# Kernel optimization log

Measured on AMD Instinct MI355X. Metric: run time of the kernel, lower is better.

The kernel has to match this reference:

```python
import jax, jax.numpy as jnp
import numpy as np
import math

N_NODES = 100000
N_EDGES = 1600000
IN_CH = 128
EDGE_DIM = 8
HEADS = 4
C1, C2 = 10, 5  # per-head out channels of conv1/conv2
N_GRAPHS = 64


def setup_inputs() -> dict:
    key = jax.random.key(0)
    k = jax.random.split(key, 26)
    s = 0.05
    d1, d2 = HEADS * C1, HEADS * C2  # 40, 20
    lin = lambda kk, fi, fo: jax.random.normal(kk, (fi, fo), jnp.float32) * s
    inp = {}
    inp['x'] = jax.random.normal(k[0], (N_NODES, IN_CH), jnp.float32)
    inp['edge_index'] = jax.random.randint(k[1], (2, N_EDGES), 0, N_NODES)
    inp['edge_attr'] = jax.random.normal(k[2], (N_EDGES, EDGE_DIM), jnp.float32)
    inp['batch'] = jnp.sort(jax.random.randint(k[3], (N_NODES,), 0, N_GRAPHS))
    # conv1 params (TransformerConv: lin_query/key/value + lin_edge(no bias) + lin_skip)
    inp['Wq1'] = lin(k[4], IN_CH, d1); inp['bq1'] = jnp.zeros((d1,), jnp.float32)
    inp['Wk1'] = lin(k[5], IN_CH, d1); inp['bk1'] = jnp.zeros((d1,), jnp.float32)
    inp['Wv1'] = lin(k[6], IN_CH, d1); inp['bv1'] = jnp.zeros((d1,), jnp.float32)
    inp['We1'] = lin(k[7], EDGE_DIM, d1)
    inp['Ws1'] = lin(k[8], IN_CH, d1); inp['bs1'] = jnp.zeros((d1,), jnp.float32)
    # conv2 params
    inp['Wq2'] = lin(k[9], d1, d2); inp['bq2'] = jnp.zeros((d2,), jnp.float32)
    inp['Wk2'] = lin(k[10], d1, d2); inp['bk2'] = jnp.zeros((d2,), jnp.float32)
    inp['Wv2'] = lin(k[11], d1, d2); inp['bv2'] = jnp.zeros((d2,), jnp.float32)
    inp['We2'] = lin(k[12], EDGE_DIM, d2)
    inp['Ws2'] = lin(k[13], d1, d2); inp['bs2'] = jnp.zeros((d2,), jnp.float32)
    # MLP head
    inp['W1'] = lin(k[14], d2, 10); inp['b1'] = jnp.zeros((10,), jnp.float32)
    inp['W2'] = lin(k[15], 10, 3); inp['b2'] = jnp.zeros((3,), jnp.float32)
    return inp


def _segment_softmax(alpha, dst, n):
    # numerically stable softmax over incoming edges of each target node
    amax = jax.ops.segment_max(alpha, dst, num_segments=n)
    ex = jnp.exp(alpha - amax[dst])
    den = jax.ops.segment_sum(ex, dst, num_segments=n)
    return ex / (den[dst] + 1e-16)


def _transformer_conv(x, src, dst, eattr, Wq, bq, Wk, bk, Wv, bv, We, Ws, bs, heads, ch):
    n = x.shape[0]
    q = (x @ Wq + bq).reshape(n, heads, ch)
    k = (x @ Wk + bk).reshape(n, heads, ch)
    v = (x @ Wv + bv).reshape(n, heads, ch)
    e = (eattr @ We).reshape(-1, heads, ch)          # [E,H,C]
    kj = k[src] + e                                   # gather + edge bias
    alpha = jnp.einsum('ehc,ehc->eh', q[dst], kj) / math.sqrt(ch)
    alpha = _segment_softmax(alpha, dst, n)           # [E,H]
    msg = (v[src] + e) * alpha[:, :, None]
    out = jax.ops.segment_sum(msg, dst, num_segments=n).reshape(n, heads * ch)
    return out + x @ Ws + bs                          # root/skip connection (beta=False)


def reference(x, edge_index, edge_attr, batch, Wq1, bq1, Wk1, bk1, Wv1, bv1, We1, Ws1, bs1, Wq2, bq2, Wk2, bk2, Wv2, bv2, We2, Ws2, bs2, W1, b1, W2, b2):
    src, dst = edge_index[0], edge_index[1]
    h = jax.nn.relu(_transformer_conv(x, src, dst, edge_attr, Wq1, bq1, Wk1, bk1, Wv1, bv1, We1, Ws1, bs1, HEADS, C1))
    h = jax.nn.relu(_transformer_conv(h, src, dst, edge_attr, Wq2, bq2, Wk2, bk2, Wv2, bv2, We2, Ws2, bs2, HEADS, C2))
    # global_mean_pool
    sums = jax.ops.segment_sum(h, batch, num_segments=N_GRAPHS)
    cnt = jax.ops.segment_sum(jnp.ones((h.shape[0],), h.dtype), batch, num_segments=N_GRAPHS)
    pooled = sums / jnp.maximum(cnt, 1.0)[:, None]
    h = jax.nn.relu(pooled @ W1 + b1)
    return h @ W2 + b2
```

## Files before the change

### kernel.cpp

```cpp
#include <hip/hip_runtime.h>
#include <math.h>

typedef short bf16x8 __attribute__((ext_vector_type(8)));
typedef float f32x4 __attribute__((ext_vector_type(4)));

__device__ __forceinline__ unsigned bfr_(float f) {
    unsigned u = __float_as_uint(f);
    return (u + 0x7fffu + ((u >> 16) & 1u)) >> 16;
}
__device__ __forceinline__ unsigned pack2_(float lo, float hi) {
    return bfr_(lo) | (bfr_(hi) << 16);
}
__device__ __forceinline__ float unlo_(unsigned u) { return __uint_as_float(u << 16); }
__device__ __forceinline__ float unhi_(unsigned u) { return __uint_as_float(u & 0xffff0000u); }
__device__ __forceinline__ float bf2f_(unsigned short us) {
    return __uint_as_float((unsigned)us << 16);
}

__global__ void k_hist(const int* __restrict__ dst, int* __restrict__ deg, int E) {
    int e = blockIdx.x * 256 + threadIdx.x;
    if (e < E) atomicAdd(&deg[dst[e]], 1);
}

__global__ void k_scan1(const int* __restrict__ deg, int* __restrict__ rp,
                        int* __restrict__ bsum, int n) {
    __shared__ int sh[256];
    int t = threadIdx.x;
    int base = blockIdx.x * 1024 + t * 4;
    int v0 = (base + 0 < n) ? deg[base + 0] : 0;
    int v1 = (base + 1 < n) ? deg[base + 1] : 0;
    int v2 = (base + 2 < n) ? deg[base + 2] : 0;
    int v3 = (base + 3 < n) ? deg[base + 3] : 0;
    int ts = v0 + v1 + v2 + v3;
    sh[t] = ts;
    __syncthreads();
    for (int off = 1; off < 256; off <<= 1) {
        int x = (t >= off) ? sh[t - off] : 0;
        __syncthreads();
        sh[t] += x;
        __syncthreads();
    }
    int run = sh[t] - ts;
    if (base + 0 < n) rp[base + 0] = run;
    run += v0;
    if (base + 1 < n) rp[base + 1] = run;
    run += v1;
    if (base + 2 < n) rp[base + 2] = run;
    run += v2;
    if (base + 3 < n) rp[base + 3] = run;
    if (t == 255) bsum[blockIdx.x] = sh[255];
}

__global__ void k_scan2(int* __restrict__ bsum, int nb) {
    __shared__ int sh[256];
    int t = threadIdx.x;
    int v = (t < nb) ? bsum[t] : 0;
    sh[t] = v;
    __syncthreads();
    for (int off = 1; off < 256; off <<= 1) {
        int x = (t >= off) ? sh[t - off] : 0;
        __syncthreads();
        sh[t] += x;
        __syncthreads();
    }
    if (t < nb) bsum[t] = sh[t] - v;
}

__global__ void k_scan3(int* __restrict__ rp, const int* __restrict__ bsum,
                        int* __restrict__ cur, int n, int total) {
    int t = threadIdx.x;
    int base = blockIdx.x * 1024 + t * 4;
    int add = bsum[blockIdx.x];
    if (base + 0 < n) { rp[base + 0] += add; cur[base + 0] = 0; }
    if (base + 1 < n) { rp[base + 1] += add; cur[base + 1] = 0; }
    if (base + 2 < n) { rp[base + 2] += add; cur[base + 2] = 0; }
    if (base + 3 < n) { rp[base + 3] += add; cur[base + 3] = 0; }
    if (blockIdx.x == 0 && t == 0) rp[n] = total;
}

__global__ void k_scatter(const int* __restrict__ src, const int* __restrict__ dst,
                          const int* __restrict__ rp, int* __restrict__ cur,
                          const float4* __restrict__ ea, int* __restrict__ src_perm,
                          uint4* __restrict__ eap, int E) {
    int e = blockIdx.x * 256 + threadIdx.x;
    if (e >= E) return;
    float4 a = ea[(size_t)e * 2 + 0];
    float4 b = ea[(size_t)e * 2 + 1];
    uint4 u;
    u.x = pack2_(a.x, a.y);
    u.y = pack2_(a.z, a.w);
    u.z = pack2_(b.x, b.y);
    u.w = pack2_(b.z, b.w);
    int d = dst[e];
    int pos = rp[d] + atomicAdd(&cur[d], 1);
    src_perm[pos] = src[e];
    eap[pos] = u;
}

__global__ void k_wprep(const float* __restrict__ Wq, const float* __restrict__ Wk,
                        const float* __restrict__ Wv, const float* __restrict__ Ws,
                        short* __restrict__ wpackT) {
    int i = blockIdx.x * 256 + threadIdx.x;
    if (i >= 160 * 136) return;
    int c = i / 136, k = i % 136;
    short v = 0;
    if (k < 128) {
        const float* W = c < 40 ? Wq : c < 80 ? Wk : c < 120 ? Wv : Ws;
        v = (short)bfr_(W[k * 40 + (c % 40)]);
    }
    wpackT[i] = v;
}

__global__ __launch_bounds__(256) void k_proj1m(
    const float* __restrict__ X, const short* __restrict__ wpackT,
    const float* __restrict__ bq, const float* __restrict__ bk,
    const float* __restrict__ bv, const float* __restrict__ bs,
    unsigned short* __restrict__ qO, unsigned* __restrict__ kvO,
    unsigned short* __restrict__ sO, int N) {
    __shared__ short xs[64 * 136];
    __shared__ short wt[160 * 136];
    int t = threadIdx.x;
    int nb = blockIdx.x * 64;
    for (int i = t; i < 64 * 32; i += 256) {
        int nl = i >> 5, k4 = (i & 31) * 4;
        int node = nb + nl;
        float4 val = make_float4(0.f, 0.f, 0.f, 0.f);
        if (node < N) val = *(const float4*)(X + (size_t)node * 128 + k4);
        uint2 pk;
        pk.x = pack2_(val.x, val.y);
        pk.y = pack2_(val.z, val.w);
        *(uint2*)(xs + nl * 136 + k4) = pk;
    }
    {
        const uint4* wsrc = (const uint4*)wpackT;
        uint4* wdst = (uint4*)wt;
        for (int i = t; i < 2720; i += 256) wdst[i] = wsrc[i];
    }
    __syncthreads();
    int wv = t >> 6;
    int lane = t & 63;
    int lrow = lane & 15;
    int kgrp = lane >> 4;
    bf16x8 afr[4];
    const short* xbase = xs + (wv * 16 + lrow) * 136;
#pragma unroll
    for (int kk = 0; kk < 4; ++kk)
        afr[kk] = *(const bf16x8*)(xbase + kk * 32 + kgrp * 8);
    f32x4 acc[10];
#pragma unroll
    for (int nt = 0; nt < 10; ++nt) acc[nt] = (f32x4){0.f, 0.f, 0.f, 0.f};
#pragma unroll
    for (int nt = 0; nt < 10; ++nt) {
        const short* wbase = wt + (nt * 16 + lrow) * 136;
#pragma unroll
        for (int kk = 0; kk < 4; ++kk) {
            bf16x8 bfr8 = *(const bf16x8*)(wbase + kk * 32 + kgrp * 8);
            acc[nt] = __builtin_amdgcn_mfma_f32_16x16x32_bf16(afr[kk], bfr8, acc[nt],
                                                              0, 0, 0);
        }
    }
    __syncthreads();
    float* cs = (float*)wt;
#pragma unroll
    for (int nt = 0; nt < 10; ++nt)
#pragma unroll
        for (int r = 0; r < 4; ++r)
            cs[(wv * 16 + kgrp * 4 + r) * 160 + nt * 16 + lrow] = acc[nt][r];
    __syncthreads();
    for (int i = t; i < 64 * 40; i += 256) {
        int nl = i / 40, c = i % 40;
        int node = nb + nl;
        if (node < N) {
            const float* row = cs + nl * 160;
            int hh = c / 10, cc = c % 10;
            float qv = row[c] + bq[c];
            float kf = row[40 + c] + bk[c];
            float vf = row[80 + c] + bv[c];
            float sv = row[120 + c] + bs[c];
            qO[(size_t)node * 64 + hh * 16 + cc] = (unsigned short)bfr_(qv);
            kvO[(size_t)node * 64 + hh * 16 + cc] = pack2_(kf, vf);
            sO[(size_t)node * 40 + c] = (unsigned short)bfr_(sv);
        }
    }
}

template <int FIN, int CH, int KTILE, int NPT, int KVP, int QP, int NPB>
__global__ __launch_bounds__(256) void k_proj(
    const float* __restrict__ X,
    const float* __restrict__ Wq, const float* __restrict__ Wk,
    const float* __restrict__ Wv, const float* __restrict__ Ws,
    const float* __restrict__ bq, const float* __restrict__ bk,
    const float* __restrict__ bv, const float* __restrict__ bs,
    unsigned short* __restrict__ qO, unsigned* __restrict__ kvO,
    unsigned short* __restrict__ sO, int N) {
    constexpr int FOUT = 4 * CH;
    constexpr int COLS = 4 * FOUT;
    constexpr int NCG = COLS / 10;
    constexpr int NG = 256 / NCG;
    static_assert(NG * NPT == NPB, "geometry");
    constexpr int F4 = FIN / 4;
    __shared__ float xs[FIN * NPB];
    __shared__ float wbuf[KTILE * COLS];
    int t = threadIdx.x;
    int nb = blockIdx.x * NPB;
    for (int i = t; i < NPB * F4; i += 256) {
        int nl = i % NPB;
        int k4 = (i / NPB) * 4;
        int node = nb + nl;
        float4 val = make_float4(0.f, 0.f, 0.f, 0.f);
        if (node < N) val = *(const float4*)(X + (size_t)node * FIN + k4);
        xs[(k4 + 0) * NPB + nl] = val.x;
        xs[(k4 + 1) * NPB + nl] = val.y;
        xs[(k4 + 2) * NPB + nl] = val.z;
        xs[(k4 + 3) * NPB + nl] = val.w;
    }
    int cg = t % NCG, ng = t / NCG;
    int which = (cg * 10) / FOUT, cc0 = (cg * 10) % FOUT;
    float acc[NPT][10];
#pragma unroll
    for (int i = 0; i < NPT; ++i)
#pragma unroll
        for (int j = 0; j < 10; ++j) acc[i][j] = 0.f;

    for (int kt = 0; kt < FIN; kt += KTILE) {
        __syncthreads();
        for (int i = t; i < KTILE * (COLS / 4); i += 256) {
            int kk = i / (COLS / 4);
            int c4 = (i % (COLS / 4)) * 4;
            int wh = c4 / FOUT, cc = c4 % FOUT;
            const float* Wsrc = wh == 0 ? Wq : wh == 1 ? Wk : wh == 2 ? Wv : Ws;
            float4 wv = *(const float4*)(Wsrc + (size_t)(kt + kk) * FOUT + cc);
            wbuf[kk * COLS + c4 + 0] = wv.x;
            wbuf[kk * COLS + c4 + 1] = wv.y;
            wbuf[kk * COLS + c4 + 2] = wv.z;
            wbuf[kk * COLS + c4 + 3] = wv.w;
        }
        __syncthreads();
#pragma unroll 4
        for (int kk = 0; kk < KTILE; ++kk) {
            float xv[NPT];
            if constexpr (NPT == 4) {
                float4 x4 = *(const float4*)(xs + (kt + kk) * NPB + ng * 4);
                xv[0] = x4.x; xv[1] = x4.y; xv[2] = x4.z; xv[3] = x4.w;
            } else if constexpr (NPT == 2) {
                float2 x2 = *(const float2*)(xs + (kt + kk) * NPB + ng * 2);
                xv[0] = x2.x; xv[1] = x2.y;
            } else {
                xv[0] = xs[(kt + kk) * NPB + ng];
            }
            const float2* wp = (const float2*)(wbuf + kk * COLS + cg * 10);
            float wv[10];
#pragma unroll
            for (int jj = 0; jj < 5; ++jj) {
                float2 w2 = wp[jj];
                wv[2 * jj] = w2.x;
                wv[2 * jj + 1] = w2.y;
            }
#pragma unroll
            for (int i = 0; i < NPT; ++i)
#pragma unroll
                for (int j = 0; j < 10; ++j) acc[i][j] += xv[i] * wv[j];
        }
    }
    const float* B = which == 0 ? bq : which == 1 ? bk : which == 2 ? bv : bs;
    float bias[10];
#pragma unroll
    for (int j = 0; j < 10; ++j) bias[j] = B[cc0 + j];
    __syncthreads();
    if (which == 0) {
#pragma unroll
        for (int i = 0; i < NPT; ++i) {
            int node = nb + ng * NPT + i;
            if (node < N)
#pragma unroll
                for (int j = 0; j < 10; ++j) {
                    int col = cc0 + j, hh = col / CH, cc = col % CH;
                    qO[(size_t)node * 4 * QP + hh * QP + cc] =
                        (unsigned short)bfr_(acc[i][j] + bias[j]);
                }
        }
    } else if (which == 3) {
#pragma unroll
        for (int i = 0; i < NPT; ++i) {
            int node = nb + ng * NPT + i;
            if (node < N)
#pragma unroll
                for (int j = 0; j < 10; ++j)
                    sO[(size_t)node * FOUT + cc0 + j] =
                        (unsigned short)bfr_(acc[i][j] + bias[j]);
        }
    } else if (which == 1) {
#pragma unroll
        for (int i = 0; i < NPT; ++i) {
            int nl = ng * NPT + i;
#pragma unroll
            for (int j = 0; j < 10; ++j) wbuf[nl * FOUT + cc0 + j] = acc[i][j] + bias[j];
        }
    }
    __syncthreads();
    if (which == 2) {
#pragma unroll
        for (int i = 0; i < NPT; ++i) {
            int nl = ng * NPT + i;
            int node = nb + nl;
            if (node < N)
#pragma unroll
                for (int j = 0; j < 10; ++j) {
                    int col = cc0 + j, hh = col / CH, cc = col % CH;
                    float kf = wbuf[nl * FOUT + cc0 + j];
                    kvO[(size_t)node * 4 * KVP + hh * KVP + cc] =
                        pack2_(kf, acc[i][j] + bias[j]);
                }
        }
    }
}

template <int CH, int KVP, int QP>
__global__ __launch_bounds__(256) void k_conv(
    const int* __restrict__ rp, const int* __restrict__ src_perm,
    const uint4* __restrict__ eap, const float* __restrict__ We,
    const unsigned short* __restrict__ qbf, const unsigned* __restrict__ kv,
    const unsigned short* __restrict__ skp, float* __restrict__ hout,
    float inv_sqrt, int N) {
    constexpr int D = 4 * CH;
    constexpr int NQL = (QP * 2) / 16;
    constexpr int NKL = KVP / 4;
    __shared__ float we_s[8 * D];
    for (int i = threadIdx.x; i < 8 * D; i += 256) we_s[i] = We[i];
    __syncthreads();
    int g = blockIdx.x * 256 + threadIdx.x;
    int node = g >> 4;
    int h = g & 3;
    int qtr = (g >> 2) & 3;
    if (node >= N) return;
    int rs = rp[node], re = rp[node + 1];
    unsigned short q16[8 * NQL];
    {
        const uint4* qp = (const uint4*)(qbf + (size_t)node * 4 * QP + h * QP);
#pragma unroll
        for (int i = 0; i < NQL; ++i) *(uint4*)&q16[8 * i] = qp[i];
    }
    float qh[CH];
#pragma unroll
    for (int c = 0; c < CH; ++c) qh[c] = bf2f_(q16[c]);
    float qe[8];
#pragma unroll
    for (int j = 0; j < 8; ++j) {
        float sE = 0.f;
#pragma unroll
        for (int c = 0; c < CH; ++c) sE += qh[c] * we_s[j * D + h * CH + c];
        qe[j] = sE;
    }
    float m = -3.0e38f, l = 0.f;
    float accv[CH] = {};
    float acce[8] = {};
    for (int p = rs + qtr; p < re; p += 4) {
        int sidx = src_perm[p];
        uint4 eu = eap[p];
        float ea8[8];
        ea8[0] = unlo_(eu.x); ea8[1] = unhi_(eu.x);
        ea8[2] = unlo_(eu.y); ea8[3] = unhi_(eu.y);
        ea8[4] = unlo_(eu.z); ea8[5] = unhi_(eu.z);
        ea8[6] = unlo_(eu.w); ea8[7] = unhi_(eu.w);
        unsigned kraw[4 * NKL];
        const uint4* kp = (const uint4*)(kv + (size_t)sidx * 4 * KVP + h * KVP);
#pragma unroll
        for (int i = 0; i < NKL; ++i) *(uint4*)&kraw[4 * i] = kp[i];
        float a = 0.f;
        float vj[CH];
#pragma unroll
        for (int c = 0; c < CH; ++c) {
            unsigned u = kraw[c];
            a += qh[c] * unlo_(u);
            vj[c] = unhi_(u);
        }
#pragma unroll
        for (int j = 0; j < 8; ++j) a += qe[j] * ea8[j];
        a *= inv_sqrt;
        float mn = fmaxf(m, a);
        float so = __expf(m - mn);
        float w = __expf(a - mn);
        l = l * so + w;
#pragma unroll
        for (int c = 0; c < CH; ++c) accv[c] = accv[c] * so + w * vj[c];
#pragma unroll
        for (int j = 0; j < 8; ++j) acce[j] = acce[j] * so + w * ea8[j];
        m = mn;
    }
#pragma unroll
    for (int mask = 4; mask <= 8; mask <<= 1) {
        float mo = __shfl_xor(m, mask);
        float lo = __shfl_xor(l, mask);
        float mn = fmaxf(m, mo);
        float s1 = (m > -1e37f) ? __expf(m - mn) : 0.f;
        float s2 = (mo > -1e37f) ? __expf(mo - mn) : 0.f;
        l = l * s1 + lo * s2;
#pragma unroll
        for (int c = 0; c < CH; ++c) {
            float ao = __shfl_xor(accv[c], mask);
            accv[c] = accv[c] * s1 + ao * s2;
        }
#pragma unroll
        for (int j = 0; j < 8; ++j) {
            float ao = __shfl_xor(acce[j], mask);
            acce[j] = acce[j] * s1 + ao * s2;
        }
        m = mn;
    }
    if (qtr == 0) {
        float inv = 1.0f / (l + 1e-16f);
#pragma unroll
        for (int c = 0; c < CH; ++c) {
            float ec = 0.f;
#pragma unroll
            for (int j = 0; j < 8; ++j) ec += acce[j] * we_s[j * D + h * CH + c];
            float o = (accv[c] + ec) * inv + bf2f_(skp[(size_t)node * D + h * CH + c]);
            hout[(size_t)node * D + h * CH + c] = fmaxf(o, 0.f);
        }
    }
}

__global__ void k_pool(const float* __restrict__ h2, const int* __restrict__ batch,
                       float* __restrict__ pooled, float* __restrict__ cnt, int N) {
    int t = blockIdx.x * 256 + threadIdx.x;
    int start = t * 16;
    if (start >= N) return;
    int end = min(start + 16, N);
    float acc[20];
#pragma unroll
    for (int c = 0; c < 20; ++c) acc[c] = 0.f;
    int cg = batch[start];
    float run = 0.f;
    for (int n = start; n < end; ++n) {
        int g = batch[n];
        if (g != cg) {
#pragma unroll
            for (int c = 0; c < 20; ++c) atomicAdd(&pooled[cg * 20 + c], acc[c]);
            atomicAdd(&cnt[cg], run);
#pragma unroll
            for (int c = 0; c < 20; ++c) acc[c] = 0.f;
            run = 0.f;
            cg = g;
        }
#pragma unroll
        for (int c = 0; c < 20; ++c) acc[c] += h2[(size_t)n * 20 + c];
        run += 1.f;
    }
#pragma unroll
    for (int c = 0; c < 20; ++c) atomicAdd(&pooled[cg * 20 + c], acc[c]);
    atomicAdd(&cnt[cg], run);
}

__global__ void k_mlp(const float* __restrict__ pooled, const float* __restrict__ cnt,
                      const float* __restrict__ W1, const float* __restrict__ b1,
                      const float* __restrict__ W2, const float* __restrict__ b2,
                      float* __restrict__ out) {
    int g = threadIdx.x;
    if (g >= 64) return;
    float ic = 1.0f / fmaxf(cnt[g], 1.0f);
    float p[20];
#pragma unroll
    for (int i = 0; i < 20; ++i) p[i] = pooled[g * 20 + i] * ic;
    float hid[10];
#pragma unroll
    for (int j = 0; j < 10; ++j) {
        float a = b1[j];
#pragma unroll
        for (int i = 0; i < 20; ++i) a += p[i] * W1[i * 10 + j];
        hid[j] = fmaxf(a, 0.f);
    }
#pragma unroll
    for (int o = 0; o < 3; ++o) {
        float a = b2[o];
#pragma unroll
        for (int j = 0; j < 10; ++j) a += hid[j] * W2[j * 3 + o];
        out[g * 3 + o] = a;
    }
}

extern "C" void kernel_launch(void* const* d_in, const int* in_sizes, int n_in,
                              void* d_out, int out_size, void* d_ws, size_t ws_size,
                              hipStream_t stream) {
    const float* x   = (const float*)d_in[0];
    const int* ei    = (const int*)d_in[1];
    const float* ea  = (const float*)d_in[2];
    const int* batch = (const int*)d_in[3];
    const float *Wq1 = (const float*)d_in[4],  *bq1 = (const float*)d_in[5];
    const float *Wk1 = (const float*)d_in[6],  *bk1 = (const float*)d_in[7];
    const float *Wv1 = (const float*)d_in[8],  *bv1 = (const float*)d_in[9];
    const float *We1 = (const float*)d_in[10];
    const float *Ws1 = (const float*)d_in[11], *bs1 = (const float*)d_in[12];
    const float *Wq2 = (const float*)d_in[13], *bq2 = (const float*)d_in[14];
    const float *Wk2 = (const float*)d_in[15], *bk2 = (const float*)d_in[16];
    const float *Wv2 = (const float*)d_in[17], *bv2 = (const float*)d_in[18];
    const float *We2 = (const float*)d_in[19];
    const float *Ws2 = (const float*)d_in[20], *bs2 = (const float*)d_in[21];
    const float *W1  = (const float*)d_in[22], *b1  = (const float*)d_in[23];
    const float *W2  = (const float*)d_in[24], *b2  = (const float*)d_in[25];

    const int N = in_sizes[0] / 128;
    const int E = in_sizes[1] / 2;
    const int* srcI = ei;
    const int* dstI = ei + E;

    float* F = (float*)d_ws;
    unsigned short* qbf = (unsigned short*)F;
    unsigned*       kv  = (unsigned*)(F + 3200000);
    float*          h1  = F + 9600000;
    float*          h2  = F + 9600000;
    unsigned short* s_bf = (unsigned short*)(F + 13600000);
    uint4*          eap = (uint4*)(F + 15600000);
    int*       src_perm = (int*)(F + 22000000);
    int* I = (int*)(F + 23600000);
    int* deg  = I;
    int* cur  = I;
    int* rpR  = I + 100352;
    int* bsum = I + 200704;
    short* wpackT = (short*)(F + 23900000);
    float* pooled = F + 23950000;
    float* cnt    = pooled + 1280;

    const int SCAN_BLOCKS = (N + 1023) / 1024;
    const int EB = (E + 255) / 256;

    hipMemsetAsync(deg, 0, (size_t)N * 4, stream);
    hipMemsetAsync(pooled, 0, (1280 + 64) * 4, stream);

    k_wprep<<<(160 * 136 + 255) / 256, 256, 0, stream>>>(Wq1, Wk1, Wv1, Ws1, wpackT);
    k_hist<<<EB, 256, 0, stream>>>(dstI, deg, E);
    k_scan1<<<SCAN_BLOCKS, 256, 0, stream>>>(deg, rpR, bsum, N);
    k_scan2<<<1, 256, 0, stream>>>(bsum, SCAN_BLOCKS);
    k_scan3<<<SCAN_BLOCKS, 256, 0, stream>>>(rpR, bsum, cur, N, E);
    k_scatter<<<EB, 256, 0, stream>>>(srcI, dstI, rpR, cur, (const float4*)ea,
                                      src_perm, eap, E);

    k_proj1m<<<(N + 63) / 64, 256, 0, stream>>>(x, wpackT, bq1, bk1, bv1, bs1,
                                                qbf, kv, s_bf, N);
    k_conv<10, 16, 16><<<(16 * N + 255) / 256, 256, 0, stream>>>(
        rpR, src_perm, eap, We1, qbf, kv, s_bf, h1, 0.31622776601683794f, N);

    k_proj<40, 5, 40, 1, 8, 8, 32><<<(N + 31) / 32, 256, 0, stream>>>(
        h1, Wq2, Wk2, Wv2, Ws2, bq2, bk2, bv2, bs2, qbf, kv, s_bf, N);
    k_conv<5, 8, 8><<<(16 * N + 255) / 256, 256, 0, stream>>>(
        rpR, src_perm, eap, We2, qbf, kv, s_bf, h2, 0.4472135954999579f, N);

    k_pool<<<((N + 15) / 16 + 255) / 256, 256, 0, stream>>>(h2, batch, pooled, cnt, N);
    k_mlp<<<1, 64, 0, stream>>>(pooled, cnt, W1, b1, W2, b2, (float*)d_out);
}
```

Measured before the change: 468.4 us.

## Replace direct CSR scatter with two-pass bucketed scatter for locality

Edges are first scattered into coarse buckets of 128 destination nodes, each split into 8 sub-buckets by block index to spread atomic contention. A second pass moves each bucket into its final CSR position, so writes to src_perm and eap stay within a small address window. The goal is to replace the random 16-byte writes and scattered atomics of the old single-pass scatter with more cache-friendly traffic. In exchange it adds an extra histogram, a single-block scan, a staging buffer and a second read/write pass over all edges.

```diff
diff --git a/kernel.cpp b/kernel.cpp
--- a/kernel.cpp
+++ b/kernel.cpp
@@ -17,9 +17,13 @@
     return __uint_as_float((unsigned)us << 16);
 }
 
-__global__ void k_hist(const int* __restrict__ dst, int* __restrict__ deg, int E) {
+__global__ void k_hist12(const int* __restrict__ dst, int* __restrict__ deg,
+                         int* __restrict__ c2, int E) {
     int e = blockIdx.x * 256 + threadIdx.x;
-    if (e < E) atomicAdd(&deg[dst[e]], 1);
+    if (e >= E) return;
+    int d = dst[e];
+    atomicAdd(&deg[d], 1);
+    atomicAdd(&c2[(d >> 7) * 8 + (blockIdx.x & 7)], 1);
 }
 
 __global__ void k_scan1(const int* __restrict__ deg, int* __restrict__ rp,
@@ -78,12 +82,41 @@
     if (blockIdx.x == 0 && t == 0) rp[n] = total;
 }
 
-__global__ void k_scatter(const int* __restrict__ src, const int* __restrict__ dst,
-                          const int* __restrict__ rp, int* __restrict__ cur,
-                          const float4* __restrict__ ea, int* __restrict__ src_perm,
-                          uint4* __restrict__ eap, int E) {
+__global__ __launch_bounds__(256) void k_scanB(const int* __restrict__ c2,
+                                               int* __restrict__ base2,
+                                               int* __restrict__ cur2, int NC, int E) {
+    __shared__ int sh[256];
+    int t = threadIdx.x;
+    int per = (NC + 255) / 256;
+    int lo = t * per, hi = min(lo + per, NC);
+    int s = 0;
+    for (int i = lo; i < hi; ++i) s += c2[i];
+    sh[t] = s;
+    __syncthreads();
+    for (int off = 1; off < 256; off <<= 1) {
+        int x = (t >= off) ? sh[t - off] : 0;
+        __syncthreads();
+        sh[t] += x;
+        __syncthreads();
+    }
+    int run = sh[t] - s;
+    for (int i = lo; i < hi; ++i) {
+        base2[i] = run;
+        run += c2[i];
+        cur2[i] = 0;
+    }
+    if (t == 255) base2[NC] = E;
+}
+
+__global__ void k_scatB(const int* __restrict__ src, const int* __restrict__ dst,
+                        const float4* __restrict__ ea, const int* __restrict__ base2,
+                        int* __restrict__ cur2,
+                        unsigned long long* __restrict__ st_se,
+                        uint4* __restrict__ st_ea, int E) {
     int e = blockIdx.x * 256 + threadIdx.x;
     if (e >= E) return;
+    int d = dst[e];
+    int key = (d >> 7) * 8 + (blockIdx.x & 7);
     float4 a = ea[(size_t)e * 2 + 0];
     float4 b = ea[(size_t)e * 2 + 1];
     uint4 u;
@@ -91,10 +124,26 @@
     u.y = pack2_(a.z, a.w);
     u.z = pack2_(b.x, b.y);
     u.w = pack2_(b.z, b.w);
-    int d = dst[e];
-    int pos = rp[d] + atomicAdd(&cur[d], 1);
-    src_perm[pos] = src[e];
-    eap[pos] = u;
+    int pos = base2[key] + atomicAdd(&cur2[key], 1);
+    st_se[pos] = ((unsigned long long)(unsigned)d << 32) | (unsigned)src[e];
+    st_ea[pos] = u;
+}
+
+__global__ __launch_bounds__(256) void k_scatC(
+    const unsigned long long* __restrict__ st_se, const uint4* __restrict__ st_ea,
+    const int* __restrict__ base2, const int* __restrict__ rp, int* __restrict__ cur,
+    int* __restrict__ src_perm, uint4* __restrict__ eap) {
+    int b = blockIdx.x;
+    int s0 = base2[b * 8];
+    int s1 = base2[b * 8 + 8];
+    for (int i = s0 + threadIdx.x; i < s1; i += 256) {
+        unsigned long long se = st_se[i];
+        int d = (int)(se >> 32);
+        int srcv = (int)(unsigned)se;
+        int pos = rp[d] + atomicAdd(&cur[d], 1);
+        src_perm[pos] = srcv;
+        eap[pos] = st_ea[i];
+    }
 }
 
 __global__ void k_wprep(const float* __restrict__ Wq, const float* __restrict__ Wk,
@@ -511,28 +560,37 @@
     unsigned short* s_bf = (unsigned short*)(F + 13600000);
     uint4*          eap = (uint4*)(F + 15600000);
     int*       src_perm = (int*)(F + 22000000);
+    unsigned long long* st_se = (unsigned long long*)F;
+    uint4*              st_ea = (uint4*)(F + 3200000);
     int* I = (int*)(F + 23600000);
-    int* deg  = I;
-    int* cur  = I;
-    int* rpR  = I + 100352;
-    int* bsum = I + 200704;
+    int* deg   = I;
+    int* cur   = I;
+    int* c2    = I + 100352;
+    int* rpR   = I + 106752;
+    int* bsum  = I + 207360;
+    int* base2 = I + 207616;
+    int* cur2  = I + 214080;
     short* wpackT = (short*)(F + 23900000);
     float* pooled = F + 23950000;
     float* cnt    = pooled + 1280;
 
     const int SCAN_BLOCKS = (N + 1023) / 1024;
     const int EB = (E + 255) / 256;
-
-    hipMemsetAsync(deg, 0, (size_t)N * 4, stream);
+    const int NBK = (N + 127) >> 7;
+    const int NC = NBK * 8;
+
+    hipMemsetAsync(deg, 0, (size_t)(100352 + 6400) * 4, stream);
     hipMemsetAsync(pooled, 0, (1280 + 64) * 4, stream);
 
     k_wprep<<<(160 * 136 + 255) / 256, 256, 0, stream>>>(Wq1, Wk1, Wv1, Ws1, wpackT);
-    k_hist<<<EB, 256, 0, stream>>>(dstI, deg, E);
+    k_hist12<<<EB, 256, 0, stream>>>(dstI, deg, c2, E);
     k_scan1<<<SCAN_BLOCKS, 256, 0, stream>>>(deg, rpR, bsum, N);
     k_scan2<<<1, 256, 0, stream>>>(bsum, SCAN_BLOCKS);
     k_scan3<<<SCAN_BLOCKS, 256, 0, stream>>>(rpR, bsum, cur, N, E);
-    k_scatter<<<EB, 256, 0, stream>>>(srcI, dstI, rpR, cur, (const float4*)ea,
-                                      src_perm, eap, E);
+    k_scanB<<<1, 256, 0, stream>>>(c2, base2, cur2, NC, E);
+    k_scatB<<<EB, 256, 0, stream>>>(srcI, dstI, (const float4*)ea, base2, cur2,
+                                    st_se, st_ea, E);
+    k_scatC<<<NBK, 256, 0, stream>>>(st_se, st_ea, base2, rpR, cur, src_perm, eap);
 
     k_proj1m<<<(N + 63) / 64, 256, 0, stream>>>(x, wpackT, bq1, bk1, bv1, bs1,
                                                 qbf, kv, s_bf, N);
```

Result: slower. 600.4 us (+28.2%).
